# Kernel tuning notes

Measured on AMD Instinct MI355X. Metric: run time of the kernel, lower is better.

## Reference

```python
import jax, jax.numpy as jnp
import numpy as np

DIM = 1024
N_HEADS = 16
HD = DIM // N_HEADS


def setup_inputs() -> dict:
    key = jax.random.key(0)
    k1, k2, k3 = jax.random.split(key, 3)
    x = jax.random.normal(k1, (4, 2048, DIM), dtype=jnp.float32)
    # torch nn.Linear weights: W_qkv [3*dim, dim], W_proj [dim, dim]; y = x @ W.T
    W_qkv = jax.random.normal(k2, (3 * DIM, DIM), dtype=jnp.float32) * 0.02
    W_proj = jax.random.normal(k3, (DIM, DIM), dtype=jnp.float32) * 0.02
    return {"x": x, "W_qkv": W_qkv, "W_proj": W_proj}


def reference(x, W_qkv, W_proj):
    B, T, D = x.shape
    H, hd = N_HEADS, HD
    # fused QKV projection: (B,T,3D)
    qkv = jnp.einsum('btd,ed->bte', x, W_qkv)
    # view(B,T,3,H,hd).transpose(1,2) -> (B,3,T,H,hd)
    qkv = qkv.reshape(B, T, 3, H, hd).transpose(0, 2, 1, 3, 4)
    q, k, v = qkv[:, 0], qkv[:, 1], qkv[:, 2]  # each (B,T,H,hd)
    # NOTE: faithful to source — SDPA sees (B,T) as batch dims and attends
    # over the heads axis (length H), NOT the sequence axis.
    scale = 1.0 / np.sqrt(hd).astype(np.float32)
    scores = jnp.einsum('btie,btje->btij', q, k) * scale  # (B,T,H,H)
    attn = jax.nn.softmax(scores, axis=-1)
    out = jnp.einsum('btij,btje->btie', attn, v)  # (B,T,H,hd)
    # out.transpose(1,2).contiguous().view(B,T,D)
    out = out.transpose(0, 2, 1, 3).reshape(B, T, D)
    return jnp.einsum('btd,ed->bte', out, W_proj)
```

## Files before the change

kernel.cpp:

```cpp
#include <hip/hip_runtime.h>


typedef __bf16 bf16x8 __attribute__((ext_vector_type(8)));
typedef float  f32x16 __attribute__((ext_vector_type(16)));
typedef float  f32x4  __attribute__((ext_vector_type(4)));

typedef __attribute__((address_space(3))) void       lds_void;
typedef const __attribute__((address_space(1))) void gbl_void;

__device__ __forceinline__ unsigned short f2b(float f) {
    unsigned int u = __builtin_bit_cast(unsigned int, f);
    return (unsigned short)((u + 0x7FFFu + ((u >> 16) & 1u)) >> 16);
}
__device__ __forceinline__ unsigned int pack2(float a, float b) {
    return (unsigned int)f2b(a) | ((unsigned int)f2b(b) << 16);
}
__device__ __forceinline__ void unpack8(uint4 u, float* f) {
    unsigned int w[4] = {u.x, u.y, u.z, u.w};
#pragma unroll
    for (int a = 0; a < 4; ++a) {
        union { unsigned int i; float f; } lo, hi;
        lo.i = w[a] << 16;
        hi.i = w[a] & 0xFFFF0000u;
        f[a * 2]     = lo.f;
        f[a * 2 + 1] = hi.f;
    }
}

__global__ __launch_bounds__(256) void cvt_all(const float* __restrict__ x,
                                               const float* __restrict__ wqkv,
                                               const float* __restrict__ wproj,
                                               unsigned short* __restrict__ xb,
                                               unsigned short* __restrict__ wqkvb,
                                               unsigned short* __restrict__ wprojb) {
    int i = blockIdx.x * 256 + threadIdx.x;
    const float* src;
    unsigned short* dst;
    if (i < 2097152)      { src = x;     dst = xb;                   }
    else if (i < 2883584) { src = wqkv;  dst = wqkvb;  i -= 2097152; }
    else                  { src = wproj; dst = wprojb; i -= 2883584; }
    float4 f = reinterpret_cast<const float4*>(src)[i];
    ushort4 u;
    u.x = f2b(f.x); u.y = f2b(f.y); u.z = f2b(f.z); u.w = f2b(f.w);
    reinterpret_cast<ushort4*>(dst)[i] = u;
}

__device__ __forceinline__ void store_c(float* C, long idx, float v)          { C[idx] = v; }
__device__ __forceinline__ void store_c(unsigned short* C, long idx, float v) { C[idx] = f2b(v); }

#define BAR   __builtin_amdgcn_s_barrier()
#define LGKM0 asm volatile("s_waitcnt lgkmcnt(0)" ::: "memory")
#define LGKM8 asm volatile("s_waitcnt lgkmcnt(8)" ::: "memory")
#define VM4   asm volatile("s_waitcnt vmcnt(4)" ::: "memory")

template <typename CT>
__global__ __launch_bounds__(512, 2) void gemm256p(const unsigned short* __restrict__ A,
                                                   const unsigned short* __restrict__ B,
                                                   CT* __restrict__ C,
                                                   int M, int N, int K, int NBX) {
    __shared__ __align__(16) unsigned short sA[2][16384];
    __shared__ __align__(16) unsigned short sB[2][16384];

    const int tid  = threadIdx.x;
    const int lane = tid & 63;
    const int wave = tid >> 6;
    const int wm   = wave >> 2;
    const int wn   = wave & 3;

    const int nwg = gridDim.x;
    const int cpx = nwg >> 3;
    const int swz = (blockIdx.x & 7) * cpx + (blockIdx.x >> 3);
    const long bm = swz / NBX;
    const long bn = swz % NBX;

    const unsigned short* Ab = A + bm * 256 * (long)K;
    const unsigned short* Bb = B + bn * 256 * (long)K;

    f32x4 acc[8][4] = {};

    auto stage = [&](const unsigned short* __restrict__ G, unsigned short* L,
                     int tile, int half) {
        const int r = tid >> 3;
        const int c = ((tid & 7) ^ (r & 7)) << 3;
        const unsigned short* g = G + (long)(half * 128 + r) * K + (long)tile * 64 + c;
        unsigned short* l = L + half * 8192 + wave * 512;
#pragma unroll
        for (int j = 0; j < 2; ++j)
            __builtin_amdgcn_global_load_lds((gbl_void*)(g + (long)j * 64 * K),
                                             (lds_void*)(l + j * 4096), 16, 0, 0);
    };

    stage(Bb, &sB[0][0], 0, 0); stage(Bb, &sB[0][0], 0, 1);
    stage(Ab, &sA[0][0], 0, 0); stage(Ab, &sA[0][0], 0, 1);
    stage(Bb, &sB[1][0], 1, 0); stage(Bb, &sB[1][0], 1, 1);
    VM4;
    BAR;

    const int fr = lane & 15;
    const int fk = lane >> 4;
    const int sx = lane & 7;

    bf16x8 af[4][2], b01[2][2], b23[2][2];

    auto read_a4 = [&](int q, int mbase) {
#pragma unroll
        for (int mt = 0; mt < 4; ++mt) {
            const int row = wm * 128 + (mbase + mt) * 16 + fr;
#pragma unroll
            for (int h = 0; h < 2; ++h)
                af[mt][h] = *reinterpret_cast<const bf16x8*>(
                    &sA[q][row * 64 + (((h * 4 + fk) ^ sx) << 3)]);
        }
    };
    auto read_b2 = [&](int q, int nbase, bf16x8 (&bf)[2][2]) {
#pragma unroll
        for (int nt = 0; nt < 2; ++nt) {
            const int row = wn * 64 + (nbase + nt) * 16 + fr;
#pragma unroll
            for (int h = 0; h < 2; ++h)
                bf[nt][h] = *reinterpret_cast<const bf16x8*>(
                    &sB[q][row * 64 + (((h * 4 + fk) ^ sx) << 3)]);
        }
    };
    auto mmq = [&](int mbase, int nbase, bf16x8 (&bf)[2][2]) {
        __builtin_amdgcn_s_setprio(1);
#pragma unroll
        for (int mt = 0; mt < 4; ++mt)
#pragma unroll
            for (int nt = 0; nt < 2; ++nt)
#pragma unroll
                for (int h = 0; h < 2; ++h)
                    acc[mbase + mt][nbase + nt] = __builtin_amdgcn_mfma_f32_16x16x32_bf16(
                        af[mt][h], bf[nt][h], acc[mbase + mt][nbase + nt], 0, 0, 0);
        __builtin_amdgcn_s_setprio(0);
    };

    const int NITER = K >> 7;
    for (int it = 0; it < NITER; ++it) {
        const int u = it * 2;
        read_a4(0, 0); read_b2(0, 0, b01);
        stage(Ab, &sA[1][0], u + 1, 0);
        LGKM8; BAR; LGKM0; mmq(0, 0, b01); BAR;
        read_b2(0, 2, b23);
        stage(Ab, &sA[1][0], u + 1, 1);
        BAR; LGKM0; mmq(0, 2, b23); BAR;
        read_a4(0, 4);
        stage(Bb, &sB[0][0], u + 2, 0);
        BAR; LGKM0; mmq(4, 2, b23); BAR;
        stage(Bb, &sB[0][0], u + 2, 1);
        BAR; mmq(4, 0, b01); BAR;
        VM4;
        read_a4(1, 0); read_b2(1, 0, b01);
        stage(Ab, &sA[0][0], u + 2, 0);
        LGKM8; BAR; LGKM0; mmq(0, 0, b01); BAR;
        read_b2(1, 2, b23);
        stage(Ab, &sA[0][0], u + 2, 1);
        BAR; LGKM0; mmq(0, 2, b23); BAR;
        read_a4(1, 4);
        stage(Bb, &sB[1][0], u + 3, 0);
        BAR; LGKM0; mmq(4, 2, b23); BAR;
        stage(Bb, &sB[1][0], u + 3, 1);
        BAR; mmq(4, 0, b01); BAR;
        VM4;
    }

    const long mb = bm * 256 + wm * 128 + (fk << 2);
    const long nb = bn * 256 + wn * 64 + fr;
#pragma unroll
    for (int mt = 0; mt < 8; ++mt)
#pragma unroll
        for (int nt = 0; nt < 4; ++nt)
#pragma unroll
            for (int r = 0; r < 4; ++r)
                store_c(C, (mb + mt * 16 + r) * (long)N + nb + nt * 16, acc[mt][nt][r]);
}

template <int BM, int BN, typename CT>
__global__ __launch_bounds__(256) void gemm_bt(const unsigned short* __restrict__ A,
                                               const unsigned short* __restrict__ B,
                                               CT* __restrict__ C,
                                               int M, int N, int K) {
    constexpr int MI = BM / 64;
    constexpr int NJ = BN / 64;
    __shared__ __align__(16) unsigned short As[BM * 64];
    __shared__ __align__(16) unsigned short Bs[BN * 64];

    const int tid  = threadIdx.x;
    const int lane = tid & 63;
    const int wave = tid >> 6;
    const long bm  = blockIdx.y;
    const long bn  = blockIdx.x;
    const int wm   = (wave >> 1) * (BM / 2);
    const int wn   = (wave & 1) * (BN / 2);

    f32x16 acc[MI][NJ] = {};

    const unsigned short* Ab = A + bm * BM * (long)K;
    const unsigned short* Bb = B + bn * BN * (long)K;

    const int srow  = tid >> 3;
    const int sgcol = ((tid & 7) ^ (srow & 7)) << 3;

    for (int k0 = 0; k0 < K; k0 += 64) {
#pragma unroll
        for (int r = 0; r < BM / 32; ++r)
            __builtin_amdgcn_global_load_lds(
                (gbl_void*)(Ab + (long)(r * 32 + srow) * K + k0 + sgcol),
                (lds_void*)(As + (r * 256 + wave * 64) * 8), 16, 0, 0);
#pragma unroll
        for (int r = 0; r < BN / 32; ++r)
            __builtin_amdgcn_global_load_lds(
                (gbl_void*)(Bb + (long)(r * 32 + srow) * K + k0 + sgcol),
                (lds_void*)(Bs + (r * 256 + wave * 64) * 8), 16, 0, 0);
        __syncthreads();

        const int arow = lane & 31;
        const int kh   = lane >> 5;
#pragma unroll
        for (int kk = 0; kk < 4; ++kk) {
            const int c  = kk * 2 + kh;
            const int sw = (c ^ (lane & 7)) << 3;
            bf16x8 af[MI], bfr[NJ];
#pragma unroll
            for (int i = 0; i < MI; ++i)
                af[i] = *reinterpret_cast<const bf16x8*>(As + (wm + i * 32 + arow) * 64 + sw);
#pragma unroll
            for (int j = 0; j < NJ; ++j)
                bfr[j] = *reinterpret_cast<const bf16x8*>(Bs + (wn + j * 32 + arow) * 64 + sw);
#pragma unroll
            for (int i = 0; i < MI; ++i)
#pragma unroll
                for (int j = 0; j < NJ; ++j)
                    acc[i][j] = __builtin_amdgcn_mfma_f32_32x32x16_bf16(af[i], bfr[j], acc[i][j], 0, 0, 0);
        }
        __syncthreads();
    }

    const long mbase = bm * BM + wm + ((lane >> 5) << 2);
    const long nbase = bn * BN + wn + (lane & 31);
#pragma unroll
    for (int i = 0; i < MI; ++i)
#pragma unroll
        for (int j = 0; j < NJ; ++j)
#pragma unroll
            for (int r = 0; r < 16; ++r) {
                const long row = mbase + i * 32 + (r & 3) + 8 * (r >> 2);
                store_c(C, row * (long)N + nbase + j * 32, acc[i][j][r]);
            }
}

__global__ __launch_bounds__(256) void attn_rowlocal(const unsigned short* __restrict__ qkv,
                                                     unsigned short* __restrict__ out3) {
    __shared__ __align__(16) unsigned short rows[4 * 3072];
    __shared__ float attnS[4][16][17];

    const int tid  = threadIdx.x;
    const int lane = tid & 63;
    const int wave = tid >> 6;
    const int m0   = blockIdx.x * 4;

    {
        const uint4* src = reinterpret_cast<const uint4*>(qkv + (long)m0 * 3072);
        uint4* dst = reinterpret_cast<uint4*>(rows);
#pragma unroll
        for (int c = 0; c < 6; ++c) {
            const int S  = c * 256 + tid;
            const int gs = (S & ~7) | ((S & 7) ^ ((S >> 3) & 7));
            dst[S] = src[gs];
        }
    }
    __syncthreads();

    const int m = m0 + wave;
    const int b = m >> 11;
    const int t = m & 2047;
    const unsigned short* rw = rows + wave * 3072;

    const int i  = lane & 15;
    const int j0 = (lane >> 4) << 2;
    float sc[4] = {0.f, 0.f, 0.f, 0.f};
#pragma unroll
    for (int c8 = 0; c8 < 8; ++c8) {
        uint4 qu = *reinterpret_cast<const uint4*>(rw + i * 64 + ((c8 ^ (i & 7)) << 3));
        float qf[8];
        unpack8(qu, qf);
#pragma unroll
        for (int jj = 0; jj < 4; ++jj) {
            const int vi = 16 + j0 + jj;
            uint4 ku = *reinterpret_cast<const uint4*>(rw + vi * 64 + ((c8 ^ (vi & 7)) << 3));
            float kf[8];
            unpack8(ku, kf);
#pragma unroll
            for (int d = 0; d < 8; ++d) sc[jj] += qf[d] * kf[d];
        }
    }
#pragma unroll
    for (int jj = 0; jj < 4; ++jj) sc[jj] *= 0.125f;

    float mx = fmaxf(fmaxf(sc[0], sc[1]), fmaxf(sc[2], sc[3]));
    mx = fmaxf(mx, __shfl_xor(mx, 16));
    mx = fmaxf(mx, __shfl_xor(mx, 32));
    float sum = 0.f;
#pragma unroll
    for (int jj = 0; jj < 4; ++jj) { sc[jj] = __expf(sc[jj] - mx); sum += sc[jj]; }
    sum += __shfl_xor(sum, 16);
    sum += __shfl_xor(sum, 32);
    const float inv = 1.0f / sum;
#pragma unroll
    for (int jj = 0; jj < 4; ++jj) attnS[wave][i][j0 + jj] = sc[jj] * inv;
    __syncthreads();

    const int oi = lane >> 2;
    const int s0 = (lane & 3) << 4;
    const int c0 = (lane & 3) << 1;
    float o[16];
#pragma unroll
    for (int ss = 0; ss < 16; ++ss) o[ss] = 0.f;
#pragma unroll
    for (int j = 0; j < 16; ++j) {
        const float a  = attnS[wave][oi][j];
        const int   vi = 32 + j;
        uint4 v0 = *reinterpret_cast<const uint4*>(rw + vi * 64 + (((c0)     ^ (vi & 7)) << 3));
        uint4 v1 = *reinterpret_cast<const uint4*>(rw + vi * 64 + (((c0 + 1) ^ (vi & 7)) << 3));
        float vf[16];
        unpack8(v0, vf);
        unpack8(v1, vf + 8);
#pragma unroll
        for (int ss = 0; ss < 16; ++ss) o[ss] += a * vf[ss];
    }

    uint4 r0, r1;
    r0.x = pack2(o[0],  o[1]);  r0.y = pack2(o[2],  o[3]);
    r0.z = pack2(o[4],  o[5]);  r0.w = pack2(o[6],  o[7]);
    r1.x = pack2(o[8],  o[9]);  r1.y = pack2(o[10], o[11]);
    r1.z = pack2(o[12], o[13]); r1.w = pack2(o[14], o[15]);

    const long base = (long)b * (2048 * 1024)
                    + (long)(oi * 128 + (t >> 4)) * 1024
                    + 64 * (t & 15) + s0;
    *reinterpret_cast<uint4*>(out3 + base)     = r0;
    *reinterpret_cast<uint4*>(out3 + base + 8) = r1;
}

extern "C" void kernel_launch(void* const* d_in, const int* in_sizes, int n_in,
                              void* d_out, int out_size, void* d_ws, size_t ws_size,
                              hipStream_t stream) {
    const float* x     = (const float*)d_in[0];
    const float* Wqkv  = (const float*)d_in[1];
    const float* Wproj = (const float*)d_in[2];
    float* out = (float*)d_out;

    char* ws = (char*)d_ws;
    unsigned short* xb     = (unsigned short*)(ws);
    unsigned short* wqkvb  = (unsigned short*)(ws + 16777216);
    unsigned short* wprojb = (unsigned short*)(ws + 23068672);
    unsigned short* qkvb   = (unsigned short*)(ws + 25165824);
    unsigned short* out3b  = (unsigned short*)(ws + 75497472);

    cvt_all<<<dim3(12288), dim3(256), 0, stream>>>(x, Wqkv, Wproj, xb, wqkvb, wprojb);

    gemm256p<unsigned short><<<dim3(384), dim3(512), 0, stream>>>(
        xb, wqkvb, qkvb, 8192, 3072, 1024, 12);

    attn_rowlocal<<<dim3(2048), dim3(256), 0, stream>>>(qkvb, out3b);

    gemm_bt<64, 128, float><<<dim3(8, 128), dim3(256), 0, stream>>>(
        out3b, wprojb, out, 8192, 1024, 1024);
}
```

Measured before the change: 211.7 us.

## Double-buffer LDS fragment reads in QKV GEMM to overlap with MFMA

Restructures the main loop of the 256x256 QKV GEMM so that LDS reads for the next quarter-tile's A/B fragments are issued before the MFMAs of the current quarter, using separate register sets (af_lo/af_hi, two b01 buffers). Waits on lgkmcnt and vmcnt are relaxed to partial counts so that LDS reads and global-to-LDS staging can proceed alongside the matrix ops. This raises register pressure and makes correctness depend on the exact wait counts and buffer ordering.

Measured after the change: 271.1 us. 28.0% more time.

```diff
diff --git a/kernel.cpp b/kernel.cpp
--- a/kernel.cpp
+++ b/kernel.cpp
@@ -48,16 +48,15 @@
 __device__ __forceinline__ void store_c(float* C, long idx, float v)          { C[idx] = v; }
 __device__ __forceinline__ void store_c(unsigned short* C, long idx, float v) { C[idx] = f2b(v); }
 
-#define BAR   __builtin_amdgcn_s_barrier()
-#define LGKM0 asm volatile("s_waitcnt lgkmcnt(0)" ::: "memory")
-#define LGKM8 asm volatile("s_waitcnt lgkmcnt(8)" ::: "memory")
-#define VM4   asm volatile("s_waitcnt vmcnt(4)" ::: "memory")
+#define BAR    __builtin_amdgcn_s_barrier()
+#define LGK(n) asm volatile("s_waitcnt lgkmcnt(" #n ")" ::: "memory")
+#define VMC(n) asm volatile("s_waitcnt vmcnt(" #n ")" ::: "memory")
 
 template <typename CT>
-__global__ __launch_bounds__(512, 2) void gemm256p(const unsigned short* __restrict__ A,
-                                                   const unsigned short* __restrict__ B,
-                                                   CT* __restrict__ C,
-                                                   int M, int N, int K, int NBX) {
+__global__ __launch_bounds__(512, 2) void gemm256pp(const unsigned short* __restrict__ A,
+                                                    const unsigned short* __restrict__ B,
+                                                    CT* __restrict__ C,
+                                                    int M, int N, int K, int NBX) {
     __shared__ __align__(16) unsigned short sA[2][16384];
     __shared__ __align__(16) unsigned short sB[2][16384];
 
@@ -90,78 +89,100 @@
                                              (lds_void*)(l + j * 4096), 16, 0, 0);
     };
 
+    const int fr = lane & 15;
+    const int fk = lane >> 4;
+    const int sx = lane & 7;
+
+    bf16x8 af_lo[4][2], af_hi[4][2], b01[2][2][2], b23[2][2];
+
+    auto rdA = [&](bf16x8 (&dst)[4][2], int q, int mbase) {
+#pragma unroll
+        for (int mt = 0; mt < 4; ++mt) {
+            const int row = wm * 128 + (mbase + mt) * 16 + fr;
+#pragma unroll
+            for (int h = 0; h < 2; ++h)
+                dst[mt][h] = *reinterpret_cast<const bf16x8*>(
+                    &sA[q][row * 64 + (((h * 4 + fk) ^ sx) << 3)]);
+        }
+    };
+    auto rdB = [&](bf16x8 (&dst)[2][2], int q, int nbase) {
+#pragma unroll
+        for (int nt = 0; nt < 2; ++nt) {
+            const int row = wn * 64 + (nbase + nt) * 16 + fr;
+#pragma unroll
+            for (int h = 0; h < 2; ++h)
+                dst[nt][h] = *reinterpret_cast<const bf16x8*>(
+                    &sB[q][row * 64 + (((h * 4 + fk) ^ sx) << 3)]);
+        }
+    };
+    auto mmq = [&](bf16x8 (&a)[4][2], bf16x8 (&b)[2][2], int mbase, int nbase) {
+        __builtin_amdgcn_s_setprio(1);
+#pragma unroll
+        for (int mt = 0; mt < 4; ++mt)
+#pragma unroll
+            for (int nt = 0; nt < 2; ++nt)
+#pragma unroll
+                for (int h = 0; h < 2; ++h)
+                    acc[mbase + mt][nbase + nt] = __builtin_amdgcn_mfma_f32_16x16x32_bf16(
+                        a[mt][h], b[nt][h], acc[mbase + mt][nbase + nt], 0, 0, 0);
+        __builtin_amdgcn_s_setprio(0);
+    };
+
     stage(Bb, &sB[0][0], 0, 0); stage(Bb, &sB[0][0], 0, 1);
     stage(Ab, &sA[0][0], 0, 0); stage(Ab, &sA[0][0], 0, 1);
     stage(Bb, &sB[1][0], 1, 0); stage(Bb, &sB[1][0], 1, 1);
-    VM4;
+    VMC(4);
     BAR;
-
-    const int fr = lane & 15;
-    const int fk = lane >> 4;
-    const int sx = lane & 7;
-
-    bf16x8 af[4][2], b01[2][2], b23[2][2];
-
-    auto read_a4 = [&](int q, int mbase) {
-#pragma unroll
-        for (int mt = 0; mt < 4; ++mt) {
-            const int row = wm * 128 + (mbase + mt) * 16 + fr;
-#pragma unroll
-            for (int h = 0; h < 2; ++h)
-                af[mt][h] = *reinterpret_cast<const bf16x8*>(
-                    &sA[q][row * 64 + (((h * 4 + fk) ^ sx) << 3)]);
-        }
-    };
-    auto read_b2 = [&](int q, int nbase, bf16x8 (&bf)[2][2]) {
-#pragma unroll
-        for (int nt = 0; nt < 2; ++nt) {
-            const int row = wn * 64 + (nbase + nt) * 16 + fr;
-#pragma unroll
-            for (int h = 0; h < 2; ++h)
-                bf[nt][h] = *reinterpret_cast<const bf16x8*>(
-                    &sB[q][row * 64 + (((h * 4 + fk) ^ sx) << 3)]);
-        }
-    };
-    auto mmq = [&](int mbase, int nbase, bf16x8 (&bf)[2][2]) {
-        __builtin_amdgcn_s_setprio(1);
-#pragma unroll
-        for (int mt = 0; mt < 4; ++mt)
-#pragma unroll
-            for (int nt = 0; nt < 2; ++nt)
-#pragma unroll
-                for (int h = 0; h < 2; ++h)
-                    acc[mbase + mt][nbase + nt] = __builtin_amdgcn_mfma_f32_16x16x32_bf16(
-                        af[mt][h], bf[nt][h], acc[mbase + mt][nbase + nt], 0, 0, 0);
-        __builtin_amdgcn_s_setprio(0);
-    };
+    rdB(b01[0], 0, 0);
+    rdA(af_lo, 0, 0);
 
     const int NITER = K >> 7;
     for (int it = 0; it < NITER; ++it) {
         const int u = it * 2;
-        read_a4(0, 0); read_b2(0, 0, b01);
+        rdB(b23, 0, 2);
         stage(Ab, &sA[1][0], u + 1, 0);
-        LGKM8; BAR; LGKM0; mmq(0, 0, b01); BAR;
-        read_b2(0, 2, b23);
+        BAR; LGK(4);
+        mmq(af_lo, b01[0], 0, 0);
+        BAR;
+        rdA(af_hi, 0, 4);
         stage(Ab, &sA[1][0], u + 1, 1);
-        BAR; LGKM0; mmq(0, 2, b23); BAR;
-        read_a4(0, 4);
+        BAR; LGK(8);
+        mmq(af_lo, b23, 0, 2);
+        BAR;
+        VMC(4);
+        rdB(b01[1], 1, 0);
         stage(Bb, &sB[0][0], u + 2, 0);
-        BAR; LGKM0; mmq(4, 2, b23); BAR;
+        BAR; LGK(4);
+        mmq(af_hi, b23, 4, 2);
+        BAR;
+        VMC(2);
+        rdA(af_lo, 1, 0);
         stage(Bb, &sB[0][0], u + 2, 1);
-        BAR; mmq(4, 0, b01); BAR;
-        VM4;
-        read_a4(1, 0); read_b2(1, 0, b01);
+        BAR; LGK(8);
+        mmq(af_hi, b01[0], 4, 0);
+        BAR;
+        rdB(b23, 1, 2);
         stage(Ab, &sA[0][0], u + 2, 0);
-        LGKM8; BAR; LGKM0; mmq(0, 0, b01); BAR;
-        read_b2(1, 2, b23);
+        BAR; LGK(4);
+        mmq(af_lo, b01[1], 0, 0);
+        BAR;
+        rdA(af_hi, 1, 4);
         stage(Ab, &sA[0][0], u + 2, 1);
-        BAR; LGKM0; mmq(0, 2, b23); BAR;
-        read_a4(1, 4);
+        BAR; LGK(8);
+        mmq(af_lo, b23, 0, 2);
+        BAR;
+        VMC(4);
+        rdB(b01[0], 0, 0);
         stage(Bb, &sB[1][0], u + 3, 0);
-        BAR; LGKM0; mmq(4, 2, b23); BAR;
+        BAR; LGK(4);
+        mmq(af_hi, b23, 4, 2);
+        BAR;
+        VMC(2);
+        rdA(af_lo, 0, 0);
         stage(Bb, &sB[1][0], u + 3, 1);
-        BAR; mmq(4, 0, b01); BAR;
-        VM4;
+        BAR; LGK(8);
+        mmq(af_hi, b01[1], 4, 0);
+        BAR;
     }
 
     const long mb = bm * 256 + wm * 128 + (fk << 2);
@@ -359,7 +380,7 @@
 
     cvt_all<<<dim3(12288), dim3(256), 0, stream>>>(x, Wqkv, Wproj, xb, wqkvb, wprojb);
 
-    gemm256p<unsigned short><<<dim3(384), dim3(512), 0, stream>>>(
+    gemm256pp<unsigned short><<<dim3(384), dim3(512), 0, stream>>>(
         xb, wqkvb, qkvb, 8192, 3072, 1024, 12);
 
     attn_rowlocal<<<dim3(2048), dim3(256), 0, stream>>>(qkvb, out3b);
```
